# Kernel optimization log

Measured on AMD Instinct MI355X. Metric: run time of the kernel, lower is better.

## Reference

```python
import jax, jax.numpy as jnp
import numpy as np

EPS = 1e-3       # module eps for mask normalization
LN_EPS = 1e-5    # torch LayerNorm default eps


def _layernorm(x, w, b):
    mu = jnp.mean(x, axis=-1, keepdims=True)
    var = jnp.var(x, axis=-1, keepdims=True)
    return (x - mu) * jax.lax.rsqrt(var + LN_EPS) * w + b


def setup_inputs() -> dict:
    key = jax.random.key(0)
    ks = jax.random.split(key, 8)
    N_seq, N_res, c_m, c_h, c_z = 256, 256, 256, 32, 128
    m = jax.random.normal(ks[0], (N_seq, N_res, c_m), jnp.float32)
    mask = jnp.ones((N_seq, N_res), jnp.float32)
    s_m = 1.0 / np.sqrt(c_m)
    ln_w = jnp.ones((c_m,), jnp.float32)
    ln_b = jnp.zeros((c_m,), jnp.float32)
    w1 = jax.random.normal(ks[1], (c_m, c_h), jnp.float32) * s_m
    b1 = jnp.zeros((c_h,), jnp.float32)
    w2 = jax.random.normal(ks[2], (c_m, c_h), jnp.float32) * s_m
    b2 = jnp.zeros((c_h,), jnp.float32)
    # linear_out has init='final' (zeros) in training; use small random so the
    # reference output / gradients are non-trivial for kernel testing.
    w_out = jax.random.normal(ks[3], (c_h * c_h, c_z), jnp.float32) * 0.02
    b_out = jnp.zeros((c_z,), jnp.float32)
    return {"m": m, "mask": mask, "ln_w": ln_w, "ln_b": ln_b,
            "w1": w1, "b1": b1, "w2": w2, "b2": b2,
            "w_out": w_out, "b_out": b_out}


def reference(m, mask, ln_w, ln_b, w1, b1, w2, b2, w_out, b_out):
    # m: [N_seq, N_res, c_m], mask: [N_seq, N_res]
    ln = _layernorm(m, ln_w, ln_b)
    mk = mask[..., None]                                 # [S, N, 1]
    a = (ln @ w1 + b1) * mk                              # [S, N, h]
    b = (ln @ w2 + b2) * mk                              # [S, N, h]
    a = jnp.swapaxes(a, -2, -3)                          # [N, S, h]
    b = jnp.swapaxes(b, -2, -3)                          # [N, S, h]
    # outer product mean over sequences: [N, N, h, h]
    outer = jnp.einsum('isc,jse->ijce', a, b)
    N = outer.shape[0]
    outer = outer.reshape(N, N, -1)                      # [N, N, h*h]
    out = outer @ w_out + b_out                          # [N, N, c_z]
    norm = jnp.einsum('si,sj->ij', mask, mask) + EPS     # [N, N]
    return out / norm[..., None]
```

## Files before the change

kernel.cpp:

```cpp
#include <hip/hip_runtime.h>
#include <hip/hip_bf16.h>
#include <stdint.h>

typedef __bf16 bf16x8 __attribute__((ext_vector_type(8)));
typedef float  f32x4  __attribute__((ext_vector_type(4)));
typedef float  f32x16 __attribute__((ext_vector_type(16)));
typedef __attribute__((address_space(1))) uint32_t u32_g;
typedef __attribute__((address_space(3))) uint32_t u32_l;
typedef unsigned short u16;
typedef u16 u16x4 __attribute__((ext_vector_type(4)));

__device__ __forceinline__ void gload16(const void* g, void* l) {
    __builtin_amdgcn_global_load_lds((u32_g*)g, (u32_l*)l, 16, 0, 0);
}

__device__ __forceinline__ u16 bf16bits(float v) {
    __bf16 h = (__bf16)v;
    return __builtin_bit_cast(u16, h);
}

#define WAITV(n) asm volatile("s_waitcnt vmcnt(" #n ")" ::: "memory")
#define BAR() do { __builtin_amdgcn_s_barrier(); \
                   __builtin_amdgcn_sched_barrier(0); } while (0)

__global__ __launch_bounds__(256) void k_prep(const float* __restrict__ w_out,
                                              const float* __restrict__ mask,
                                              const float* __restrict__ w1,
                                              const float* __restrict__ w2,
                                              u16* __restrict__ WT,
                                              u16* __restrict__ WcatT,
                                              float* __restrict__ rnormv) {
    __shared__ float mcol[256];
    const int b = blockIdx.x, t = threadIdx.x;
    if (b < 512) {
        int idx = b * 256 + t;
        int z = idx >> 10, kc = idx & 1023;
        int c = kc & 31, e = kc >> 5;
        WT[idx] = bf16bits(w_out[(c * 32 + e) * 128 + z]);
    } else if (b < 576) {
        int idx = (b - 512) * 256 + t;
        int n = idx >> 8, k = idx & 255;
        float v = (n < 32) ? w1[k * 32 + n] : w2[k * 32 + (n - 32)];
        WcatT[idx] = bf16bits(v);
    } else {
        int i = b - 576;
        mcol[t] = mask[(size_t)t * 256 + i];
        __syncthreads();
        float acc = 1e-3f;
#pragma unroll 8
        for (int s = 0; s < 256; ++s)
            acc += mcol[s] * mask[(size_t)s * 256 + t];
        rnormv[i * 256 + t] = 1.0f / acc;
    }
}

__global__ __launch_bounds__(256, 2) void k_lnproj(
        const float* __restrict__ M, const float* __restrict__ mask,
        const float* __restrict__ lnw, const float* __restrict__ lnb,
        const float* __restrict__ b1, const float* __restrict__ b2,
        const u16* __restrict__ WcatT,
        u16* __restrict__ AT, u16* __restrict__ BT) {
    __shared__ __align__(16) u16 sh[32768];
    const int tid = threadIdx.x, lane = tid & 63, w = tid >> 6;
    const int i = blockIdx.x, s0 = blockIdx.y * 64;

#pragma unroll
    for (int p = 0; p < 8; ++p) {
        int flat = p * 256 + tid;
        int r = flat >> 5, slot = flat & 31;
        int gs = slot ^ (r & 7);
        const char* src = (const char*)WcatT + (size_t)r * 512 + (size_t)gs * 16;
        char* dst = (char*)sh + 32768 + (size_t)(p * 256 + (tid & ~63)) * 16;
        gload16(src, dst);
    }

    float4 wv = *(const float4*)(lnw + lane * 4);
    float4 bv = *(const float4*)(lnb + lane * 4);
    float4 xv[16];
#pragma unroll
    for (int it = 0; it < 16; ++it) {
        int s = s0 + w * 16 + it;
        xv[it] = *(const float4*)(M + ((size_t)s * 256 + i) * 256 + lane * 4);
    }
#pragma unroll
    for (int it = 0; it < 16; ++it) {
        int row = w * 16 + it;
        float4 x = xv[it];
        float s1 = x.x + x.y + x.z + x.w;
        float s2 = x.x * x.x + x.y * x.y + x.z * x.z + x.w * x.w;
#pragma unroll
        for (int o = 1; o < 64; o <<= 1) {
            s1 += __shfl_xor(s1, o);
            s2 += __shfl_xor(s2, o);
        }
        float mu   = s1 * 0.00390625f;
        float var  = s2 * 0.00390625f - mu * mu;
        float rstd = rsqrtf(var + 1e-5f);
        u16x4 pk;
        pk[0] = bf16bits((x.x - mu) * rstd * wv.x + bv.x);
        pk[1] = bf16bits((x.y - mu) * rstd * wv.y + bv.y);
        pk[2] = bf16bits((x.z - mu) * rstd * wv.z + bv.z);
        pk[3] = bf16bits((x.w - mu) * rstd * wv.w + bv.w);
        int byte = (row * 512 + lane * 8) ^ ((row & 7) << 4);
        *(u16x4*)((char*)sh + byte) = pk;
    }
    __syncthreads();

    f32x4 acc[4] = {};
#pragma unroll
    for (int kk = 0; kk < 8; ++kk) {
        int kb = kk * 64 + ((lane >> 4) << 4);
        int arow = w * 16 + (lane & 15);
        bf16x8 af = *(const bf16x8*)((const char*)sh +
                     ((arow * 512 + kb) ^ ((arow & 7) << 4)));
#pragma unroll
        for (int f = 0; f < 4; ++f) {
            int nrow = f * 16 + (lane & 15);
            bf16x8 bfr = *(const bf16x8*)((const char*)sh + 32768 +
                          ((nrow * 512 + kb) ^ ((nrow & 7) << 4)));
            acc[f] = __builtin_amdgcn_mfma_f32_16x16x32_bf16(af, bfr, acc[f], 0, 0, 0);
        }
    }

    const int sb = s0 + w * 16 + ((lane >> 4) << 2);
    float mk[4];
#pragma unroll
    for (int r = 0; r < 4; ++r) mk[r] = mask[(size_t)(sb + r) * 256 + i];
#pragma unroll
    for (int f = 0; f < 4; ++f) {
        int col = f * 16 + (lane & 15);
        float bias = (col < 32) ? b1[col] : b2[col - 32];
        u16* dst = ((col < 32) ? AT : BT) + ((size_t)i * 32 + (col & 31)) * 256 + sb;
        u16x4 pk;
#pragma unroll
        for (int r = 0; r < 4; ++r)
            pk[r] = bf16bits((acc[f][r] + bias) * mk[r]);
        *(u16x4*)dst = pk;
    }
}

__global__ __launch_bounds__(512, 4) void k_fused(
        const u16* __restrict__ AT, const u16* __restrict__ BT,
        const u16* __restrict__ WT, const float* __restrict__ rnormv,
        const float* __restrict__ b_out, float* __restrict__ out) {
    __shared__ __align__(16) u16 sh[36864];
    const int tid  = threadIdx.x;
    const int lane = tid & 63;
    const int wid  = tid >> 6;
    const int wr   = wid >> 2, wc = wid & 3;
    const int l15  = lane & 15;
    const int q16  = lane >> 4;
    const int lid = blockIdx.x;
    const int x   = lid & 7;
    const int kk_ = lid >> 3;
    const int bx  = (x & 3) * 16 + (kk_ & 15);
    const int by  = (x >> 2) * 16 + (kk_ >> 4);
    const int m0 = bx * 128, n0 = by * 256;

    f32x4 acc[4][4] = {};

    auto stage = [&](int kt, int buf) {
        char* base = (char*)sh + buf * 24576;
        const int k0 = kt * 32;
        {
            int r = tid >> 2, slot = tid & 3;
            int gs = slot ^ ((r >> 1) & 3);
            gload16((const char*)AT + (((size_t)(m0 + r)) * 256 + k0) * 2 + gs * 16,
                    base + (size_t)(tid & ~63) * 16);
        }
#pragma unroll
        for (int q = 0; q < 2; ++q) {
            int flat = q * 512 + tid;
            int r = flat >> 2, slot = flat & 3;
            int gs = slot ^ ((r >> 1) & 3);
            gload16((const char*)BT + (((size_t)(n0 + r)) * 256 + k0) * 2 + gs * 16,
                    base + 8192 + (size_t)(q * 512 + (tid & ~63)) * 16);
        }
    };

    auto compute = [&](int buf) {
        const char* Ab = (const char*)sh + buf * 24576;
        const char* Bb = Ab + 8192;
        bf16x8 af[4], bfr[4];
#pragma unroll
        for (int mi = 0; mi < 4; ++mi) {
            int rA = wr * 64 + mi * 16 + l15;
            af[mi] = *(const bf16x8*)(Ab + rA * 64 + (q16 ^ ((rA >> 1) & 3)) * 16);
        }
#pragma unroll
        for (int nj = 0; nj < 4; ++nj) {
            int rB = wc * 64 + nj * 16 + l15;
            bfr[nj] = *(const bf16x8*)(Bb + rB * 64 + (q16 ^ ((rB >> 1) & 3)) * 16);
        }
        __builtin_amdgcn_s_setprio(1);
#pragma unroll
        for (int mi = 0; mi < 4; ++mi)
#pragma unroll
            for (int nj = 0; nj < 4; ++nj)
                acc[mi][nj] = __builtin_amdgcn_mfma_f32_16x16x32_bf16(
                    af[mi], bfr[nj], acc[mi][nj], 0, 0, 0);
        __builtin_amdgcn_s_setprio(0);
    };

    stage(0, 0);
    stage(1, 1);
    WAITV(3);
    BAR();
#pragma unroll
    for (int t = 0; t < 8; ++t) {
        if (t + 2 < 8) stage(t + 2, (t + 2) % 3);
        compute(t % 3);
        if (t < 6) { WAITV(3); }
        else if (t == 6) { WAITV(0); }
        BAR();
    }

#pragma unroll
    for (int mi = 0; mi < 4; ++mi)
#pragma unroll
        for (int nj = 0; nj < 4; ++nj) {
            int m = wr * 64 + mi * 16 + (q16 << 2);
            int n = wc * 64 + nj * 16 + l15;
            int pr = ((m >> 5) << 3) | (n >> 5);
            int c0 = m & 31, e = n & 31;
            int byte = pr * 2048 + (e * 32 + c0) * 2;
            byte ^= ((pr ^ e) & 7) << 4;
            u16x4 pk;
#pragma unroll
            for (int r = 0; r < 4; ++r)
                pk[r] = bf16bits(acc[mi][nj][r]);
            *(u16x4*)((char*)sh + byte) = pk;
        }
    __syncthreads();

    const int slice = wid & 3;
    const int half  = wid >> 2;
    const int z0  = slice * 32;
    const int hi  = lane >> 5;
    const int p32 = lane & 31;
    const u16* wtrow = WT + (size_t)(z0 + p32) * 1024 + half * 512 + hi * 8;

    f32x16 a0 = {}, a1 = {};
    bf16x8 wbr[8];
#pragma unroll
    for (int d = 0; d < 8; ++d)
        wbr[d] = *(const bf16x8*)(wtrow + d * 16);

    auto paddr = [&](int ks) {
        int kc = half * 512 + ks * 16 + hi * 8;
        int byte = p32 * 2048 + kc * 2;
        byte ^= ((p32 ^ (kc >> 5)) & 7) << 4;
        return (const bf16x8*)((const char*)sh + byte);
    };
    bf16x8 pa0 = *paddr(0), pa1 = *paddr(1);

#pragma unroll
    for (int ks = 0; ks < 32; ++ks) {
        bf16x8 cur = (ks & 1) ? pa1 : pa0;
        if (ks + 2 < 32) {
            if (ks & 1) pa1 = *paddr(ks + 2);
            else        pa0 = *paddr(ks + 2);
        }
        if (ks & 1)
            a1 = __builtin_amdgcn_mfma_f32_32x32x16_bf16(cur, wbr[ks & 7], a1, 0, 0, 0);
        else
            a0 = __builtin_amdgcn_mfma_f32_32x32x16_bf16(cur, wbr[ks & 7], a0, 0, 0, 0);
        if (ks + 8 < 32)
            wbr[ks & 7] = *(const bf16x8*)(wtrow + (ks + 8) * 16);
    }
#pragma unroll
    for (int r = 0; r < 16; ++r) a0[r] += a1[r];

    __syncthreads();
    float* red = (float*)sh;
    if (half == 1) {
#pragma unroll
        for (int r = 0; r < 16; ++r)
            red[slice * 1024 + r * 64 + lane] = a0[r];
    }
    __syncthreads();

    if (half == 0) {
        const int i0 = bx * 4, j0 = by * 8;
        const int z  = z0 + p32;
        const float bz = b_out[z];
#pragma unroll
        for (int r = 0; r < 16; ++r) {
            float v = a0[r] + red[slice * 1024 + r * 64 + lane];
            int pair = (r & 3) + 8 * (r >> 2) + 4 * hi;
            int i = i0 + (pair >> 3), j = j0 + (pair & 7);
            out[((size_t)(i * 256 + j)) * 128 + z] =
                (v + bz) * rnormv[i * 256 + j];
        }
    }
}

extern "C" void kernel_launch(void* const* d_in, const int* in_sizes, int n_in,
                              void* d_out, int out_size, void* d_ws, size_t ws_size,
                              hipStream_t stream) {
    const float* M    = (const float*)d_in[0];
    const float* mask = (const float*)d_in[1];
    const float* lnw  = (const float*)d_in[2];
    const float* lnb  = (const float*)d_in[3];
    const float* w1   = (const float*)d_in[4];
    const float* b1   = (const float*)d_in[5];
    const float* w2   = (const float*)d_in[6];
    const float* b2   = (const float*)d_in[7];
    const float* wout = (const float*)d_in[8];
    const float* bout = (const float*)d_in[9];
    float* out = (float*)d_out;

    char* ws = (char*)d_ws;
    u16*   AT    = (u16*)(ws);
    u16*   BT    = (u16*)(ws + 4194304);
    u16*   WT    = (u16*)(ws + 8388608);
    float* rnormv= (float*)(ws + 8650752);
    u16*   WcatT = (u16*)(ws + 8912896);

    k_prep  <<<832, 256, 0, stream>>>(wout, mask, w1, w2, WT, WcatT, rnormv);
    k_lnproj<<<dim3(256, 4), 256, 0, stream>>>(M, mask, lnw, lnb, b1, b2, WcatT, AT, BT);
    k_fused <<<2048, 512, 0, stream>>>(AT, BT, WT, rnormv, bout, out);
}
```

Baseline: 118.2 us.

## Keep A tile resident in LDS and loop over four B column groups per block

Each block now loads its full 128x256 A slab into LDS once and iterates over four 256-wide B column groups, so the grid shrinks from 2048 to 512 blocks. B is double-buffered instead of triple-buffered, and the next group's first B tile is prefetched during the epilogue. The aim is to stop re-fetching A for every output tile. In exchange, LDS use grows to 128 KB and occupancy drops to 2 blocks per CU. There is also less pipelining depth and a full wait on every k-step.

```diff
diff --git a/kernel.cpp b/kernel.cpp
--- a/kernel.cpp
+++ b/kernel.cpp
@@ -139,11 +139,11 @@
     }
 }
 
-__global__ __launch_bounds__(512, 4) void k_fused(
+__global__ __launch_bounds__(512, 2) void k_fused(
         const u16* __restrict__ AT, const u16* __restrict__ BT,
         const u16* __restrict__ WT, const float* __restrict__ rnormv,
         const float* __restrict__ b_out, float* __restrict__ out) {
-    __shared__ __align__(16) u16 sh[36864];
+    __shared__ __align__(16) u16 sh[65536];
     const int tid  = threadIdx.x;
     const int lane = tid & 63;
     const int wid  = tid >> 6;
@@ -154,144 +154,155 @@
     const int x   = lid & 7;
     const int kk_ = lid >> 3;
     const int bx  = (x & 3) * 16 + (kk_ & 15);
-    const int by  = (x >> 2) * 16 + (kk_ >> 4);
-    const int m0 = bx * 128, n0 = by * 256;
-
-    f32x4 acc[4][4] = {};
-
-    auto stage = [&](int kt, int buf) {
-        char* base = (char*)sh + buf * 24576;
-        const int k0 = kt * 32;
-        {
-            int r = tid >> 2, slot = tid & 3;
-            int gs = slot ^ ((r >> 1) & 3);
-            gload16((const char*)AT + (((size_t)(m0 + r)) * 256 + k0) * 2 + gs * 16,
-                    base + (size_t)(tid & ~63) * 16);
-        }
+    const int bg  = (x >> 2) * 4 + (kk_ >> 4);
+    const int m0  = bx * 128;
+
+    auto stageA = [&]() {
+#pragma unroll
+        for (int p = 0; p < 8; ++p) {
+            int flat = p * 512 + tid;
+            int r = flat >> 5, slot = flat & 31;
+            int gs = slot ^ (r & 7);
+            gload16((const char*)AT + (size_t)(m0 + r) * 512 + (size_t)gs * 16,
+                    (char*)sh + (size_t)(p * 512 + (tid & ~63)) * 16);
+        }
+    };
+    auto stageB = [&](int g, int t, int buf) {
+        const int n0 = (bg * 4 + g) * 256;
+        const int k0 = t * 32;
+        char* base = (char*)sh + 65536 + buf * 16384;
 #pragma unroll
         for (int q = 0; q < 2; ++q) {
             int flat = q * 512 + tid;
             int r = flat >> 2, slot = flat & 3;
             int gs = slot ^ ((r >> 1) & 3);
             gload16((const char*)BT + (((size_t)(n0 + r)) * 256 + k0) * 2 + gs * 16,
-                    base + 8192 + (size_t)(q * 512 + (tid & ~63)) * 16);
+                    base + (size_t)(q * 512 + (tid & ~63)) * 16);
         }
     };
 
-    auto compute = [&](int buf) {
-        const char* Ab = (const char*)sh + buf * 24576;
-        const char* Bb = Ab + 8192;
-        bf16x8 af[4], bfr[4];
-#pragma unroll
-        for (int mi = 0; mi < 4; ++mi) {
-            int rA = wr * 64 + mi * 16 + l15;
-            af[mi] = *(const bf16x8*)(Ab + rA * 64 + (q16 ^ ((rA >> 1) & 3)) * 16);
-        }
-#pragma unroll
-        for (int nj = 0; nj < 4; ++nj) {
-            int rB = wc * 64 + nj * 16 + l15;
-            bfr[nj] = *(const bf16x8*)(Bb + rB * 64 + (q16 ^ ((rB >> 1) & 3)) * 16);
-        }
-        __builtin_amdgcn_s_setprio(1);
+    stageA();
+    stageB(0, 0, 0);
+    WAITV(0);
+    BAR();
+
+#pragma unroll 1
+    for (int g = 0; g < 4; ++g) {
+        f32x4 acc[4][4] = {};
+
+#pragma unroll
+        for (int t = 0; t < 8; ++t) {
+            if (t < 7) stageB(g, t + 1, (t + 1) & 1);
+            {
+                const char* Ab = (const char*)sh;
+                const char* Bb = (const char*)sh + 65536 + (t & 1) * 16384;
+                bf16x8 af[4], bfr[4];
+#pragma unroll
+                for (int mi = 0; mi < 4; ++mi) {
+                    int rA = wr * 64 + mi * 16 + l15;
+                    int slotI = (t * 4 + q16) ^ (rA & 7);
+                    af[mi] = *(const bf16x8*)(Ab + rA * 512 + slotI * 16);
+                }
+#pragma unroll
+                for (int nj = 0; nj < 4; ++nj) {
+                    int rB = wc * 64 + nj * 16 + l15;
+                    bfr[nj] = *(const bf16x8*)(Bb + rB * 64 +
+                               (q16 ^ ((rB >> 1) & 3)) * 16);
+                }
+                __builtin_amdgcn_s_setprio(1);
+#pragma unroll
+                for (int mi = 0; mi < 4; ++mi)
+#pragma unroll
+                    for (int nj = 0; nj < 4; ++nj)
+                        acc[mi][nj] = __builtin_amdgcn_mfma_f32_16x16x32_bf16(
+                            af[mi], bfr[nj], acc[mi][nj], 0, 0, 0);
+                __builtin_amdgcn_s_setprio(0);
+            }
+            WAITV(0);
+            BAR();
+        }
+
 #pragma unroll
         for (int mi = 0; mi < 4; ++mi)
 #pragma unroll
-            for (int nj = 0; nj < 4; ++nj)
-                acc[mi][nj] = __builtin_amdgcn_mfma_f32_16x16x32_bf16(
-                    af[mi], bfr[nj], acc[mi][nj], 0, 0, 0);
-        __builtin_amdgcn_s_setprio(0);
-    };
-
-    stage(0, 0);
-    stage(1, 1);
-    WAITV(3);
-    BAR();
-#pragma unroll
-    for (int t = 0; t < 8; ++t) {
-        if (t + 2 < 8) stage(t + 2, (t + 2) % 3);
-        compute(t % 3);
-        if (t < 6) { WAITV(3); }
-        else if (t == 6) { WAITV(0); }
-        BAR();
-    }
-
-#pragma unroll
-    for (int mi = 0; mi < 4; ++mi)
-#pragma unroll
-        for (int nj = 0; nj < 4; ++nj) {
-            int m = wr * 64 + mi * 16 + (q16 << 2);
-            int n = wc * 64 + nj * 16 + l15;
-            int pr = ((m >> 5) << 3) | (n >> 5);
-            int c0 = m & 31, e = n & 31;
-            int byte = pr * 2048 + (e * 32 + c0) * 2;
-            byte ^= ((pr ^ e) & 7) << 4;
-            u16x4 pk;
-#pragma unroll
-            for (int r = 0; r < 4; ++r)
-                pk[r] = bf16bits(acc[mi][nj][r]);
-            *(u16x4*)((char*)sh + byte) = pk;
-        }
-    __syncthreads();
-
-    const int slice = wid & 3;
-    const int half  = wid >> 2;
-    const int z0  = slice * 32;
-    const int hi  = lane >> 5;
-    const int p32 = lane & 31;
-    const u16* wtrow = WT + (size_t)(z0 + p32) * 1024 + half * 512 + hi * 8;
-
-    f32x16 a0 = {}, a1 = {};
-    bf16x8 wbr[8];
-#pragma unroll
-    for (int d = 0; d < 8; ++d)
-        wbr[d] = *(const bf16x8*)(wtrow + d * 16);
-
-    auto paddr = [&](int ks) {
-        int kc = half * 512 + ks * 16 + hi * 8;
-        int byte = p32 * 2048 + kc * 2;
-        byte ^= ((p32 ^ (kc >> 5)) & 7) << 4;
-        return (const bf16x8*)((const char*)sh + byte);
-    };
-    bf16x8 pa0 = *paddr(0), pa1 = *paddr(1);
-
-#pragma unroll
-    for (int ks = 0; ks < 32; ++ks) {
-        bf16x8 cur = (ks & 1) ? pa1 : pa0;
-        if (ks + 2 < 32) {
-            if (ks & 1) pa1 = *paddr(ks + 2);
-            else        pa0 = *paddr(ks + 2);
-        }
-        if (ks & 1)
-            a1 = __builtin_amdgcn_mfma_f32_32x32x16_bf16(cur, wbr[ks & 7], a1, 0, 0, 0);
-        else
-            a0 = __builtin_amdgcn_mfma_f32_32x32x16_bf16(cur, wbr[ks & 7], a0, 0, 0, 0);
-        if (ks + 8 < 32)
-            wbr[ks & 7] = *(const bf16x8*)(wtrow + (ks + 8) * 16);
-    }
-#pragma unroll
-    for (int r = 0; r < 16; ++r) a0[r] += a1[r];
-
-    __syncthreads();
-    float* red = (float*)sh;
-    if (half == 1) {
-#pragma unroll
-        for (int r = 0; r < 16; ++r)
-            red[slice * 1024 + r * 64 + lane] = a0[r];
-    }
-    __syncthreads();
-
-    if (half == 0) {
-        const int i0 = bx * 4, j0 = by * 8;
-        const int z  = z0 + p32;
-        const float bz = b_out[z];
-#pragma unroll
-        for (int r = 0; r < 16; ++r) {
-            float v = a0[r] + red[slice * 1024 + r * 64 + lane];
-            int pair = (r & 3) + 8 * (r >> 2) + 4 * hi;
-            int i = i0 + (pair >> 3), j = j0 + (pair & 7);
-            out[((size_t)(i * 256 + j)) * 128 + z] =
-                (v + bz) * rnormv[i * 256 + j];
-        }
+            for (int nj = 0; nj < 4; ++nj) {
+                int m = wr * 64 + mi * 16 + (q16 << 2);
+                int n = wc * 64 + nj * 16 + l15;
+                int pr = ((m >> 5) << 3) | (n >> 5);
+                int c0 = m & 31, e = n & 31;
+                int byte = pr * 2048 + (e * 32 + c0) * 2;
+                byte ^= ((pr ^ e) & 7) << 4;
+                u16x4 pk;
+#pragma unroll
+                for (int r = 0; r < 4; ++r)
+                    pk[r] = bf16bits(acc[mi][nj][r]);
+                *(u16x4*)((char*)sh + 65536 + byte) = pk;
+            }
+        __syncthreads();
+
+        const int slice = wid & 3;
+        const int half  = wid >> 2;
+        const int z0  = slice * 32;
+        const int hi  = lane >> 5;
+        const int p32 = lane & 31;
+        const u16* wtrow = WT + (size_t)(z0 + p32) * 1024 + half * 512 + hi * 8;
+
+        f32x16 a0 = {}, a1 = {};
+        bf16x8 wbr[8];
+#pragma unroll
+        for (int d = 0; d < 8; ++d)
+            wbr[d] = *(const bf16x8*)(wtrow + d * 16);
+
+        auto paddr = [&](int ks) {
+            int kc = half * 512 + ks * 16 + hi * 8;
+            int byte = p32 * 2048 + kc * 2;
+            byte ^= ((p32 ^ (kc >> 5)) & 7) << 4;
+            return (const bf16x8*)((const char*)sh + 65536 + byte);
+        };
+        bf16x8 pa0 = *paddr(0), pa1 = *paddr(1);
+
+#pragma unroll
+        for (int ks = 0; ks < 32; ++ks) {
+            bf16x8 cur = (ks & 1) ? pa1 : pa0;
+            if (ks + 2 < 32) {
+                if (ks & 1) pa1 = *paddr(ks + 2);
+                else        pa0 = *paddr(ks + 2);
+            }
+            if (ks & 1)
+                a1 = __builtin_amdgcn_mfma_f32_32x32x16_bf16(cur, wbr[ks & 7], a1, 0, 0, 0);
+            else
+                a0 = __builtin_amdgcn_mfma_f32_32x32x16_bf16(cur, wbr[ks & 7], a0, 0, 0, 0);
+            if (ks + 8 < 32)
+                wbr[ks & 7] = *(const bf16x8*)(wtrow + (ks + 8) * 16);
+        }
+#pragma unroll
+        for (int r = 0; r < 16; ++r) a0[r] += a1[r];
+
+        __syncthreads();
+        if (g < 3) stageB(g + 1, 0, 0);
+
+        float* red = (float*)((char*)sh + 98304);
+        if (half == 1) {
+#pragma unroll
+            for (int r = 0; r < 16; ++r)
+                red[slice * 1024 + r * 64 + lane] = a0[r];
+        }
+        __syncthreads();
+
+        if (half == 0) {
+            const int i0 = bx * 4, j0 = (bg * 4 + g) * 8;
+            const int z  = z0 + p32;
+            const float bz = b_out[z];
+#pragma unroll
+            for (int r = 0; r < 16; ++r) {
+                float v = a0[r] + red[slice * 1024 + r * 64 + lane];
+                int pair = (r & 3) + 8 * (r >> 2) + 4 * hi;
+                int i = i0 + (pair >> 3), j = j0 + (pair & 7);
+                out[((size_t)(i * 256 + j)) * 128 + z] =
+                    (v + bz) * rnormv[i * 256 + j];
+            }
+        }
+        if (g < 3) { WAITV(0); BAR(); }
     }
 }
 
@@ -319,5 +330,5 @@
 
     k_prep  <<<832, 256, 0, stream>>>(wout, mask, w1, w2, WT, WcatT, rnormv);
     k_lnproj<<<dim3(256, 4), 256, 0, stream>>>(M, mask, lnw, lnb, b1, b2, WcatT, AT, BT);
-    k_fused <<<2048, 512, 0, stream>>>(AT, BT, WT, rnormv, bout, out);
-}
+    k_fused <<<512, 512, 0, stream>>>(AT, BT, WT, rnormv, bout, out);
+}
```

Measured after the change: 133.4 us. 1.13x slower.
